# Performance work log

Measured on AMD Instinct MI355X. Metric: run time of the kernel, lower is better.

The kernel has to match this reference:

```python
import jax, jax.numpy as jnp
import numpy as np

WL_W = 8   # wl_weight
WL_IN = 8  # wl_activate (input quantization)
EPS = 1e-5

def _wq(x, bits):
    # WAGE-style uniform quantize-dequantize to `bits` bits in [-1+step, 1-step], STE passthrough
    step = 2.0 ** (1 - bits)
    q = jnp.clip(jnp.round(x / step) * step, -1.0 + step, 1.0 - step)
    return x + jax.lax.stop_gradient(q - x)

def _qconv(x, w, b, pad):
    y = jax.lax.conv_general_dilated(
        _wq(x, WL_IN), _wq(w, WL_W), (1, 1), [(pad, pad), (pad, pad)],
        dimension_numbers=('NCHW', 'OIHW', 'NCHW'))
    return y + b[None, :, None, None]

def _bn_relu(x, g, be):
    # BatchNorm2d in training mode: batch statistics over (N, H, W)
    m = jnp.mean(x, axis=(0, 2, 3), keepdims=True)
    v = jnp.var(x, axis=(0, 2, 3), keepdims=True)
    return jax.nn.relu((x - m) * jax.lax.rsqrt(v + EPS) * g[None, :, None, None] + be[None, :, None, None])

def _maxpool3(x):
    # MaxPool2d(3, stride=1, padding=1)
    return jax.lax.reduce_window(x, -jnp.inf, jax.lax.max,
                                 (1, 1, 3, 3), (1, 1, 1, 1),
                                 [(0, 0), (0, 0), (1, 1), (1, 1)])

def setup_inputs() -> dict:
    key = jax.random.key(0)
    ks = jax.random.split(key, 8)
    d = {'x': jax.random.normal(ks[0], (128, 192, 32, 32), jnp.float32)}
    specs = [('b1', 1, 64, 192, 1), ('b2a', 2, 96, 192, 1), ('b2b', 3, 128, 96, 3),
             ('b3a', 4, 16, 192, 1), ('b3b', 5, 32, 16, 3), ('b3c', 6, 32, 32, 3),
             ('b4', 7, 32, 192, 1)]
    for name, i, co, ci, k in specs:
        d[name + '_w'] = jax.random.normal(ks[i], (co, ci, k, k), jnp.float32) * 0.05
        d[name + '_b'] = jnp.zeros((co,), jnp.float32)
        d[name + '_g'] = jnp.ones((co,), jnp.float32)
        d[name + '_be'] = jnp.zeros((co,), jnp.float32)
    return d

def reference(x,
              b1_w, b1_b, b1_g, b1_be,
              b2a_w, b2a_b, b2a_g, b2a_be,
              b2b_w, b2b_b, b2b_g, b2b_be,
              b3a_w, b3a_b, b3a_g, b3a_be,
              b3b_w, b3b_b, b3b_g, b3b_be,
              b3c_w, b3c_b, b3c_g, b3c_be,
              b4_w, b4_b, b4_g, b4_be):
    y1 = _bn_relu(_qconv(x, b1_w, b1_b, 0), b1_g, b1_be)
    y2 = _bn_relu(_qconv(x, b2a_w, b2a_b, 0), b2a_g, b2a_be)
    y2 = _bn_relu(_qconv(y2, b2b_w, b2b_b, 1), b2b_g, b2b_be)
    y3 = _bn_relu(_qconv(x, b3a_w, b3a_b, 0), b3a_g, b3a_be)
    y3 = _bn_relu(_qconv(y3, b3b_w, b3b_b, 1), b3b_g, b3b_be)
    y3 = _bn_relu(_qconv(y3, b3c_w, b3c_b, 1), b3c_g, b3c_be)
    y4 = _bn_relu(_qconv(_maxpool3(x), b4_w, b4_b, 0), b4_g, b4_be)
    return jnp.concatenate([y1, y2, y3, y4], axis=1)  # [N, 256, 32, 32]
```

## Files before the change

kernel.cpp:

```cpp
#include <hip/hip_runtime.h>

typedef unsigned short u16;
typedef unsigned int u32;
typedef __attribute__((ext_vector_type(4))) int i32x4;
typedef __attribute__((ext_vector_type(4))) float f32x4;
typedef __attribute__((ext_vector_type(4))) u16 u16x4;
typedef __attribute__((ext_vector_type(8))) u16 u16x8;

#define PTOT 131072
#define NREP 16

static __device__ __forceinline__ int qi8(float v) {
  int q = (int)rintf(v * 128.f);
  return max(-127, min(127, q));
}
static __device__ __forceinline__ u16 bf_rne(float v) {
  u32 u = __float_as_uint(v);
  u += 0x7fffu + ((u >> 16) & 1u);
  return (u16)(u >> 16);
}
static __device__ __forceinline__ float bf2f(u16 v) {
  return __uint_as_float((u32)v << 16);
}

struct WPtrs { const float* p[7]; };

__global__ void wpack_kernel(WPtrs wp, char* __restrict__ o) {
  static const int S[7][5] = {
      {0,      192, 192, 1, 64},
      {12288,  192, 192, 1, 96},
      {30720,  96,  320, 3, 128},
      {153600, 192, 192, 1, 16},
      {156672, 16,  64,  3, 32},
      {162816, 32,  128, 3, 32},
      {175104, 192, 192, 1, 32},
  };
  int idx = blockIdx.x * 256 + threadIdx.x;
  if (idx >= 181248) return;
  int s = 0;
#pragma unroll
  for (int i = 1; i < 7; ++i)
    if (idx >= S[i][0]) s = i;
  int local = idx - S[s][0];
  int CIr = S[s][1], KROWP = S[s][2], KH = S[s][3], Co = S[s][4];
  int j = local & 15, lane = (local >> 4) & 63, f = local >> 10;
  int NF = Co >> 4;
  int c = f / NF, nf = f - c * NF;
  int co = nf * 16 + (lane & 15);
  int k = c * 64 + ((lane >> 4) << 4) + j;
  int r = k / KROWP, kk = k - r * KROWP;
  char val = 0;
  if (kk < 3 * CIr || KH == 1) {
    int kw = (KH == 1) ? 0 : (kk / CIr);
    int ci = (KH == 1) ? kk : (kk - kw * CIr);
    val = (char)qi8(wp.p[s][(((size_t)co * CIr + ci) * KH + r) * KH + kw]);
  }
  o[idx] = val;
}

__global__ __launch_bounds__(256) void quantx_kernel(const float* __restrict__ x,
                                                     char* __restrict__ xq) {
  __shared__ __align__(16) char tile[64][80];
  int n = blockIdx.z, hwb = blockIdx.x * 64, cb = blockIdx.y * 64;
  int lane = threadIdx.x & 63, sub = threadIdx.x >> 6;
#pragma unroll
  for (int i = 0; i < 16; ++i) {
    int c = sub + i * 4;
    float v = x[(((size_t)n * 192 + cb + c) << 10) + hwb + lane];
    tile[lane][c] = (char)qi8(v);
  }
  __syncthreads();
  int t = threadIdx.x, px = t >> 2, c16 = t & 3;
  uint4 v = *(const uint4*)&tile[px][c16 * 16];
  *(uint4*)&xq[(((size_t)n << 10) + hwb + px) * 192 + cb + c16 * 16] = v;
}

__global__ __launch_bounds__(256) void pool_kernel(const char* __restrict__ xq,
                                                   char* __restrict__ xpq) {
  int idx = blockIdx.x * 256 + threadIdx.x;
  int c16 = idx % 12;
  int p = idx / 12;
  int n = p >> 10, hw = p & 1023, h = hw >> 5, w = hw & 31;
  int m[16];
#pragma unroll
  for (int j = 0; j < 16; ++j) m[j] = -127;
  for (int dh = -1; dh <= 1; ++dh) {
    int hh = h + dh; if (hh < 0 || hh > 31) continue;
    for (int dw = -1; dw <= 1; ++dw) {
      int ww = w + dw; if (ww < 0 || ww > 31) continue;
      uint4 v = *(const uint4*)&xq[((((size_t)n << 5) + hh) * 32 + ww) * 192 + c16 * 16];
      const char* bb = reinterpret_cast<const char*>(&v);
#pragma unroll
      for (int t = 0; t < 16; ++t) {
        int b = (int)bb[t];
        m[t] = b > m[t] ? b : m[t];
      }
    }
  }
  uint4 o;
  char* ob = reinterpret_cast<char*>(&o);
#pragma unroll
  for (int t = 0; t < 16; ++t) ob[t] = (char)m[t];
  *(uint4*)&xpq[(size_t)p * 192 + c16 * 16] = o;
}

template <int NFW, int MF>
static __device__ __forceinline__ void conv_epilogue(
    i32x4 (&acc)[MF][NFW], int nfw, int lane, int wave, int mbase,
    u16* __restrict__ yh, double* __restrict__ stb, int ststride) {
  float yv[MF][NFW][4];
#pragma unroll
  for (int mf = 0; mf < MF; ++mf)
#pragma unroll
    for (int nf = 0; nf < NFW; ++nf)
      if (nf < nfw) {
        int col = nf * 16 + (lane & 15);
        int pix = mbase + mf * 16 + ((lane >> 4) << 2);
        u16x4 o;
#pragma unroll
        for (int r = 0; r < 4; ++r) {
          float v = (float)acc[mf][nf][r] * 6.103515625e-05f;
          yv[mf][nf][r] = v;
          o[r] = bf_rne(v);
        }
        *(u16x4*)&yh[(size_t)col * PTOT + pix] = o;
      }

  float s1[NFW], s2[NFW];
#pragma unroll
  for (int nf = 0; nf < NFW; ++nf) { s1[nf] = 0.f; s2[nf] = 0.f; }
#pragma unroll
  for (int mf = 0; mf < MF; ++mf)
#pragma unroll
    for (int nf = 0; nf < NFW; ++nf)
      if (nf < nfw)
#pragma unroll
        for (int r = 0; r < 4; ++r) {
          float v = yv[mf][nf][r];
          s1[nf] += v;
          s2[nf] += v * v;
        }
#pragma unroll
  for (int m = 16; m <= 32; m <<= 1)
#pragma unroll
    for (int nf = 0; nf < NFW; ++nf) {
      s1[nf] += __shfl_xor(s1[nf], m);
      s2[nf] += __shfl_xor(s2[nf], m);
    }
  __shared__ float red[4][NFW][16][2];
  if (lane < 16)
#pragma unroll
    for (int nf = 0; nf < NFW; ++nf) {
      red[wave][nf][lane][0] = s1[nf];
      red[wave][nf][lane][1] = s2[nf];
    }
  __syncthreads();
  const int t = threadIdx.x;
  if (t < 16 * nfw) {
    int nf = t >> 4, l = t & 15;
    float a = red[0][nf][l][0] + red[1][nf][l][0] + red[2][nf][l][0] + red[3][nf][l][0];
    float b = red[0][nf][l][1] + red[1][nf][l][1] + red[2][nf][l][1] + red[3][nf][l][1];
    int rep = blockIdx.x & (NREP - 1);
    atomicAdd(&stb[rep * ststride + 2 * t], (double)a);
    atomicAdd(&stb[rep * ststride + 2 * t + 1], (double)b);
  }
}

__global__ __launch_bounds__(256, 4) void cstat1x1_kernel(
    const char* __restrict__ xq, const char* __restrict__ xpq,
    const char* __restrict__ bpk, double* __restrict__ st, u16* __restrict__ yh) {
  constexpr int NFW = 6;
  constexpr int MF = 2;
  __shared__ __align__(16) char btile[18432];

  const int b = blockIdx.y;
  const int nfw = (b == 0) ? 4 : (b == 1) ? 6 : (b == 2) ? 1 : 2;
  const int bpo = (b == 0) ? 0 : (b == 1) ? 12288 : (b == 2) ? 153600 : 175104;
  const int sto = (b == 0) ? 0 : (b == 1) ? 256 * NREP
                           : (b == 2) ? 3 * 256 * NREP : 6 * 256 * NREP;
  const int yho = (b == 0) ? 0 : (b == 1) ? 64 : (b == 2) ? 160 : 176;
  const char* xin = (b == 3) ? xpq : xq;
  const char* bp = bpk + bpo;
  double* stb = st + sto;
  u16* yhb = yh + (size_t)yho * PTOT;

  const int tid = threadIdx.x;
  const int bsz = nfw * 3 * 1024;
  for (int s = tid * 16; s < bsz; s += 4096)
    *(uint4*)&btile[s] = *(const uint4*)(bp + s);
  __syncthreads();

  const int lane = tid & 63;
  const int wave = tid >> 6;
  const int mbase = blockIdx.x * 128 + wave * 32;

  uint abase[MF];
#pragma unroll
  for (int mf = 0; mf < MF; ++mf)
    abase[mf] = (uint)(mbase + mf * 16 + (lane & 15)) * 192u;
  const uint klane = (uint)(lane >> 4) * 16u;
  const uint blane = (uint)lane * 16u;

  i32x4 acc[MF][NFW];
#pragma unroll
  for (int i = 0; i < MF; ++i)
#pragma unroll
    for (int j = 0; j < NFW; ++j) acc[i][j] = {0, 0, 0, 0};

#pragma unroll
  for (int c = 0; c < 3; ++c) {
    i32x4 af[MF];
#pragma unroll
    for (int mf = 0; mf < MF; ++mf)
      af[mf] = *(const i32x4*)(xin + (abase[mf] + (uint)c * 64u + klane));
    i32x4 bfr[NFW];
#pragma unroll
    for (int nf = 0; nf < NFW; ++nf)
      if (nf < nfw)
        bfr[nf] = *(const i32x4*)&btile[(uint)((c * nfw + nf) * 1024) + blane];
#pragma unroll
    for (int mf = 0; mf < MF; ++mf)
#pragma unroll
      for (int nf = 0; nf < NFW; ++nf)
        if (nf < nfw)
          acc[mf][nf] = __builtin_amdgcn_mfma_i32_16x16x64_i8(af[mf], bfr[nf],
                                                              acc[mf][nf], 0, 0, 0);
  }

  conv_epilogue<NFW, MF>(acc, nfw, lane, wave, mbase, yhb, stb, 256);
}

template <int CI, int KROWP, int COB>
__global__ __launch_bounds__(256, 4) void cstat9q_kernel(
    const u16* __restrict__ yhin, const double* __restrict__ stp,
    const float* __restrict__ gp, const float* __restrict__ bep,
    const char* __restrict__ bp, int nft,
    double* __restrict__ stb, u16* __restrict__ yh) {
  constexpr int CPR = KROWP / 64;
  constexpr int NCH = 3 * CPR;
  constexpr int NFW = COB / 16;
  constexpr int MF = 2;
  constexpr int TILE = 6 * 34 * CI;
  constexpr int BSZ = NCH * NFW * 1024;

  __shared__ __align__(16) char atile[TILE + 64];
  __shared__ __align__(16) char btile[BSZ];
  __shared__ float2 cfl[CI];

  const int tid = threadIdx.x;

  if (tid < CI) {
    double s1d = 0., s2d = 0.;
#pragma unroll
    for (int r = 0; r < NREP; ++r) {
      s1d += stp[r * 256 + 2 * tid];
      s2d += stp[r * 256 + 2 * tid + 1];
    }
    double m = s1d * (1.0 / PTOT);
    double v = s2d * (1.0 / PTOT) - m * m;
    double inv = 1.0 / sqrt(v + 1e-5);
    double c0 = (double)gp[tid] * inv;
    cfl[tid] = make_float2((float)c0, (float)((double)bep[tid] - m * c0));
  }
  for (int s = tid * 16; s < BSZ; s += 4096)
    *(uint4*)&btile[s] = *(const uint4*)(bp + s);
  {
    uint4 z = {0, 0, 0, 0};
    for (int s = tid * 16; s < TILE + 64; s += 4096) *(uint4*)&atile[s] = z;
  }
  __syncthreads();

  const int p0 = blockIdx.x * 128;
  const int n = p0 >> 10, h0 = (p0 & 1023) >> 5;
  for (int task = tid; task < CI * 6; task += 256) {
    int co = task / 6, rr = task - co * 6;
    int irow = h0 - 1 + rr;
    if (irow < 0 || irow > 31) continue;
    const u16* src = yhin + (size_t)co * PTOT + (n << 10) + (irow << 5);
    float2 cc = cfl[co];
    char* dst = &atile[(rr * 34 + 1) * CI + co];
#pragma unroll
    for (int w8 = 0; w8 < 4; ++w8) {
      u16x8 v = *(const u16x8*)(src + w8 * 8);
#pragma unroll
      for (int e = 0; e < 8; ++e) {
        float z = fmaxf(fmaf(bf2f(v[e]), cc.x, cc.y), 0.f);
        dst[(w8 * 8 + e) * CI] = (char)min((int)rintf(z * 128.f), 127);
      }
    }
  }
  __syncthreads();

  const int lane = tid & 63;
  const int wave = tid >> 6;
  const int mbase = blockIdx.x * 128 + wave * 32;

  uint albase[MF];
#pragma unroll
  for (int mf = 0; mf < MF; ++mf) {
    int lp = wave * 32 + mf * 16 + (lane & 15);
    albase[mf] = (uint)((((lp >> 5) + 1) * 34 + 1 + (lp & 31)) * CI);
  }
  const uint klane = (uint)(lane >> 4) * 16u;
  const uint blane = (uint)lane * 16u;

  i32x4 acc[MF][NFW];
#pragma unroll
  for (int i = 0; i < MF; ++i)
#pragma unroll
    for (int j = 0; j < NFW; ++j) acc[i][j] = {0, 0, 0, 0};

#pragma unroll 2
  for (int c = 0; c < NCH; ++c) {
    int rr = c / CPR, o = (c - rr * CPR) * 64;
    uint koff = (uint)((rr - 1) * 34 * CI + o - CI);
    i32x4 af[MF];
#pragma unroll
    for (int mf = 0; mf < MF; ++mf)
      af[mf] = *(const i32x4*)&atile[albase[mf] + koff + klane];
    i32x4 bfr[NFW];
#pragma unroll
    for (int nf = 0; nf < NFW; ++nf)
      bfr[nf] = *(const i32x4*)&btile[(uint)((c * nft + nf) * 1024) + blane];
#pragma unroll
    for (int mf = 0; mf < MF; ++mf)
#pragma unroll
      for (int nf = 0; nf < NFW; ++nf)
        acc[mf][nf] = __builtin_amdgcn_mfma_i32_16x16x64_i8(af[mf], bfr[nf],
                                                            acc[mf][nf], 0, 0, 0);
  }

  conv_epilogue<NFW, MF>(acc, NFW, lane, wave, mbase, yh, stb, 256);
}

__global__ __launch_bounds__(256, 3) void cstat9q2_kernel(
    const u16* __restrict__ yhin, const double* __restrict__ stp,
    const float* __restrict__ gp, const float* __restrict__ bep,
    const char* __restrict__ bp, double* __restrict__ stb, u16* __restrict__ yh) {
  constexpr int CI = 96;
  constexpr int CPR = 5;
  constexpr int NCH = 15;
  constexpr int MF = 4;
  constexpr int NFW = 4;
  constexpr int TILE = 6 * 34 * CI;

  __shared__ __align__(16) char atile[TILE + 64];
  __shared__ float2 cfl[CI];
  __shared__ float red[4][NFW][16][2];

  const int tid = threadIdx.x;

  if (tid < CI) {
    double s1d = 0., s2d = 0.;
#pragma unroll
    for (int r = 0; r < NREP; ++r) {
      s1d += stp[r * 256 + 2 * tid];
      s2d += stp[r * 256 + 2 * tid + 1];
    }
    double m = s1d * (1.0 / PTOT);
    double v = s2d * (1.0 / PTOT) - m * m;
    double inv = 1.0 / sqrt(v + 1e-5);
    double c0 = (double)gp[tid] * inv;
    cfl[tid] = make_float2((float)c0, (float)((double)bep[tid] - m * c0));
  }
  {
    uint4 z = {0, 0, 0, 0};
    for (int s = tid * 16; s < TILE + 64; s += 4096) *(uint4*)&atile[s] = z;
  }
  __syncthreads();

  const int p0 = blockIdx.x * 128;
  const int n = p0 >> 10, h0 = (p0 & 1023) >> 5;
  for (int task = tid; task < CI * 6; task += 256) {
    int co = task / 6, rr = task - co * 6;
    int irow = h0 - 1 + rr;
    if (irow < 0 || irow > 31) continue;
    const u16* src = yhin + (size_t)co * PTOT + (n << 10) + (irow << 5);
    float2 cc = cfl[co];
    char* dst = &atile[(rr * 34 + 1) * CI + co];
#pragma unroll
    for (int w8 = 0; w8 < 4; ++w8) {
      u16x8 v = *(const u16x8*)(src + w8 * 8);
#pragma unroll
      for (int e = 0; e < 8; ++e) {
        float z = fmaxf(fmaf(bf2f(v[e]), cc.x, cc.y), 0.f);
        dst[(w8 * 8 + e) * CI] = (char)min((int)rintf(z * 128.f), 127);
      }
    }
  }
  __syncthreads();

  const int lane = tid & 63;
  const int wave = tid >> 6;
  const int pg = wave >> 1, cg = wave & 1;

  uint albase[MF];
#pragma unroll
  for (int mf = 0; mf < MF; ++mf) {
    int lp = pg * 64 + mf * 16 + (lane & 15);
    albase[mf] = (uint)((((lp >> 5) + 1) * 34 + 1 + (lp & 31)) * CI);
  }
  const uint klane = (uint)(lane >> 4) * 16u;
  const uint blane = (uint)lane * 16u;

  i32x4 acc[MF][NFW];
#pragma unroll
  for (int i = 0; i < MF; ++i)
#pragma unroll
    for (int j = 0; j < NFW; ++j) acc[i][j] = {0, 0, 0, 0};

#pragma unroll 3
  for (int c = 0; c < NCH; ++c) {
    int rr = c / CPR, o = (c - rr * CPR) * 64;
    uint koff = (uint)((rr - 1) * 34 * CI + o - CI);
    i32x4 af[MF];
#pragma unroll
    for (int mf = 0; mf < MF; ++mf)
      af[mf] = *(const i32x4*)&atile[albase[mf] + koff + klane];
    i32x4 bfr[NFW];
#pragma unroll
    for (int nf = 0; nf < NFW; ++nf)
      bfr[nf] = *(const i32x4*)(bp + ((uint)((c * 8 + cg * 4 + nf) * 1024) + blane));
#pragma unroll
    for (int mf = 0; mf < MF; ++mf)
#pragma unroll
      for (int nf = 0; nf < NFW; ++nf)
        acc[mf][nf] = __builtin_amdgcn_mfma_i32_16x16x64_i8(af[mf], bfr[nf],
                                                            acc[mf][nf], 0, 0, 0);
  }

  float yv[MF][NFW][4];
#pragma unroll
  for (int mf = 0; mf < MF; ++mf)
#pragma unroll
    for (int nf = 0; nf < NFW; ++nf) {
      int col = cg * 64 + nf * 16 + (lane & 15);
      int pix = p0 + pg * 64 + mf * 16 + ((lane >> 4) << 2);
      u16x4 o;
#pragma unroll
      for (int r = 0; r < 4; ++r) {
        float v = (float)acc[mf][nf][r] * 6.103515625e-05f;
        yv[mf][nf][r] = v;
        o[r] = bf_rne(v);
      }
      *(u16x4*)&yh[(size_t)col * PTOT + pix] = o;
    }

  float s1[NFW], s2[NFW];
#pragma unroll
  for (int nf = 0; nf < NFW; ++nf) { s1[nf] = 0.f; s2[nf] = 0.f; }
#pragma unroll
  for (int mf = 0; mf < MF; ++mf)
#pragma unroll
    for (int nf = 0; nf < NFW; ++nf)
#pragma unroll
      for (int r = 0; r < 4; ++r) {
        float v = yv[mf][nf][r];
        s1[nf] += v;
        s2[nf] += v * v;
      }
#pragma unroll
  for (int m = 16; m <= 32; m <<= 1)
#pragma unroll
    for (int nf = 0; nf < NFW; ++nf) {
      s1[nf] += __shfl_xor(s1[nf], m);
      s2[nf] += __shfl_xor(s2[nf], m);
    }
  if (lane < 16)
#pragma unroll
    for (int nf = 0; nf < NFW; ++nf) {
      red[wave][nf][lane][0] = s1[nf];
      red[wave][nf][lane][1] = s2[nf];
    }
  __syncthreads();
  if (tid < 128) {
    int gch = tid >> 4, l = tid & 15;
    int cg2 = gch >> 2, nf = gch & 3;
    float a = red[cg2][nf][l][0] + red[2 + cg2][nf][l][0];
    float b = red[cg2][nf][l][1] + red[2 + cg2][nf][l][1];
    int rep = blockIdx.x & (NREP - 1);
    atomicAdd(&stb[rep * 256 + 2 * tid], (double)a);
    atomicAdd(&stb[rep * 256 + 2 * tid + 1], (double)b);
  }
}

struct BnPtrs { const float* g[4]; const float* be[4]; };

__global__ __launch_bounds__(256) void bnout_all_kernel(
    const u16* __restrict__ yh, const double* __restrict__ st, BnPtrs bp,
    float* __restrict__ out) {
  int co = blockIdx.y, chunk = blockIdx.x, tid = threadIdx.x;
  int br = (co < 64) ? 0 : (co < 192) ? 1 : (co < 224) ? 2 : 3;
  int lco = co - ((br == 0) ? 0 : (br == 1) ? 64 : (br == 2) ? 192 : 224);
  int yhoff = (br == 0) ? 0 : (br == 1) ? 208 : (br == 2) ? 368 : 176;
  int stoff = (br == 0) ? 0 : (br == 1) ? 2 * 256 * NREP
                         : (br == 2) ? 5 * 256 * NREP : 6 * 256 * NREP;
  const double* stb = st + stoff;
  double s1d = 0., s2d = 0.;
#pragma unroll
  for (int r = 0; r < NREP; ++r) {
    s1d += stb[r * 256 + 2 * lco];
    s2d += stb[r * 256 + 2 * lco + 1];
  }
  double m = s1d * (1.0 / PTOT);
  double v = s2d * (1.0 / PTOT) - m * m;
  double inv = 1.0 / sqrt(v + 1e-5);
  double c0d = (double)bp.g[br][lco] * inv;
  float c0 = (float)c0d;
  float c1 = (float)((double)bp.be[br][lco] - m * c0d);

  int p0 = chunk * 4096 + tid * 16;
  int n = p0 >> 10, hw = p0 & 1023;
  const u16* yp = yh + (size_t)(yhoff + lco) * PTOT + p0;
  float* op = out + (((size_t)(n * 256 + co)) << 10) + hw;
#pragma unroll
  for (int half = 0; half < 2; ++half) {
    u16x8 r = *(const u16x8*)(yp + half * 8);
    f32x4 a, b;
#pragma unroll
    for (int e = 0; e < 4; ++e) {
      a[e] = fmaxf(fmaf(bf2f(r[e]), c0, c1), 0.f);
      b[e] = fmaxf(fmaf(bf2f(r[e + 4]), c0, c1), 0.f);
    }
    *(f32x4*)(op + half * 8) = a;
    *(f32x4*)(op + half * 8 + 4) = b;
  }
}

extern "C" void kernel_launch(void* const* d_in, const int* in_sizes, int n_in,
                              void* d_out, int out_size, void* d_ws, size_t ws_size,
                              hipStream_t stream) {
  const float* x = (const float*)d_in[0];
  float* out = (float*)d_out;
  char* ws = (char*)d_ws;

  if (ws_size < 155599872ull) return;
  char* xq  = ws;
  char* xpq = ws + 25165824ull;
  u16* yh   = (u16*)(ws + 50331648ull);
  char* bpk = ws + 155189248ull;
  double* st = (double*)(ws + 155370496ull);

  hipMemsetAsync(st, 0, 7 * NREP * 256 * 8, stream);

  WPtrs wp;
  const int widx[7] = {1, 5, 9, 13, 17, 21, 25};
  for (int i = 0; i < 7; ++i) wp.p[i] = (const float*)d_in[widx[i]];
  wpack_kernel<<<708, 256, 0, stream>>>(wp, bpk);

  quantx_kernel<<<dim3(16, 3, 128), 256, 0, stream>>>(x, xq);
  pool_kernel<<<6144, 256, 0, stream>>>(xq, xpq);

  double* stB[7];
  for (int b = 0; b < 7; ++b) stB[b] = st + (size_t)b * NREP * 256;

  cstat1x1_kernel<<<dim3(1024, 4), 256, 0, stream>>>(xq, xpq, bpk, st, yh);

  cstat9q2_kernel<<<1024, 256, 0, stream>>>(
      yh + (size_t)64 * PTOT, stB[1], (const float*)d_in[7], (const float*)d_in[8],
      bpk + 30720, stB[2], yh + (size_t)208 * PTOT);

  cstat9q_kernel<16, 64, 32><<<1024, 256, 0, stream>>>(
      yh + (size_t)160 * PTOT, stB[3], (const float*)d_in[15], (const float*)d_in[16],
      bpk + 156672, 2, stB[4], yh + (size_t)336 * PTOT);

  cstat9q_kernel<32, 128, 32><<<1024, 256, 0, stream>>>(
      yh + (size_t)336 * PTOT, stB[4], (const float*)d_in[19], (const float*)d_in[20],
      bpk + 162816, 2, stB[5], yh + (size_t)368 * PTOT);

  BnPtrs bp;
  bp.g[0] = (const float*)d_in[3];  bp.be[0] = (const float*)d_in[4];
  bp.g[1] = (const float*)d_in[11]; bp.be[1] = (const float*)d_in[12];
  bp.g[2] = (const float*)d_in[23]; bp.be[2] = (const float*)d_in[24];
  bp.g[3] = (const float*)d_in[27]; bp.be[3] = (const float*)d_in[28];
  bnout_all_kernel<<<dim3(32, 256), 256, 0, stream>>>(yh, st, bp, out);
}
```

Before: 193.6 us.

## Fuse maxpool into branch-4 conv and merge two 3x3 convs into one launch

Removes the standalone pool kernel and its global xpq buffer: a new cpool4 kernel computes the 3x3 max-pool of the int8 input into shared memory and runs the 1x1 branch-4 conv directly from there. The 96->128 3x3 conv and the 16->32 3x3 conv are merged into one launch with blockIdx.y picking the branch, so the two independent convs run concurrently and one launch is saved. This cuts a global write and read of the pooled tensor plus launch gaps. In exchange, the pool reads neighbours redundantly from global, and the merged kernel pairs unequal workloads under one shared-memory and register budget.

```diff
diff --git a/kernel.cpp b/kernel.cpp
--- a/kernel.cpp
+++ b/kernel.cpp
@@ -75,35 +75,6 @@
   *(uint4*)&xq[(((size_t)n << 10) + hwb + px) * 192 + cb + c16 * 16] = v;
 }
 
-__global__ __launch_bounds__(256) void pool_kernel(const char* __restrict__ xq,
-                                                   char* __restrict__ xpq) {
-  int idx = blockIdx.x * 256 + threadIdx.x;
-  int c16 = idx % 12;
-  int p = idx / 12;
-  int n = p >> 10, hw = p & 1023, h = hw >> 5, w = hw & 31;
-  int m[16];
-#pragma unroll
-  for (int j = 0; j < 16; ++j) m[j] = -127;
-  for (int dh = -1; dh <= 1; ++dh) {
-    int hh = h + dh; if (hh < 0 || hh > 31) continue;
-    for (int dw = -1; dw <= 1; ++dw) {
-      int ww = w + dw; if (ww < 0 || ww > 31) continue;
-      uint4 v = *(const uint4*)&xq[((((size_t)n << 5) + hh) * 32 + ww) * 192 + c16 * 16];
-      const char* bb = reinterpret_cast<const char*>(&v);
-#pragma unroll
-      for (int t = 0; t < 16; ++t) {
-        int b = (int)bb[t];
-        m[t] = b > m[t] ? b : m[t];
-      }
-    }
-  }
-  uint4 o;
-  char* ob = reinterpret_cast<char*>(&o);
-#pragma unroll
-  for (int t = 0; t < 16; ++t) ob[t] = (char)m[t];
-  *(uint4*)&xpq[(size_t)p * 192 + c16 * 16] = o;
-}
-
 template <int NFW, int MF>
 static __device__ __forceinline__ void conv_epilogue(
     i32x4 (&acc)[MF][NFW], int nfw, int lane, int wave, int mbase,
@@ -167,19 +138,17 @@
 }
 
 __global__ __launch_bounds__(256, 4) void cstat1x1_kernel(
-    const char* __restrict__ xq, const char* __restrict__ xpq,
-    const char* __restrict__ bpk, double* __restrict__ st, u16* __restrict__ yh) {
+    const char* __restrict__ xq, const char* __restrict__ bpk,
+    double* __restrict__ st, u16* __restrict__ yh) {
   constexpr int NFW = 6;
   constexpr int MF = 2;
   __shared__ __align__(16) char btile[18432];
 
   const int b = blockIdx.y;
-  const int nfw = (b == 0) ? 4 : (b == 1) ? 6 : (b == 2) ? 1 : 2;
-  const int bpo = (b == 0) ? 0 : (b == 1) ? 12288 : (b == 2) ? 153600 : 175104;
-  const int sto = (b == 0) ? 0 : (b == 1) ? 256 * NREP
-                           : (b == 2) ? 3 * 256 * NREP : 6 * 256 * NREP;
-  const int yho = (b == 0) ? 0 : (b == 1) ? 64 : (b == 2) ? 160 : 176;
-  const char* xin = (b == 3) ? xpq : xq;
+  const int nfw = (b == 0) ? 4 : (b == 1) ? 6 : 1;
+  const int bpo = (b == 0) ? 0 : (b == 1) ? 12288 : 153600;
+  const int sto = (b == 0) ? 0 : (b == 1) ? 256 * NREP : 3 * 256 * NREP;
+  const int yho = (b == 0) ? 0 : (b == 1) ? 64 : 160;
   const char* bp = bpk + bpo;
   double* stb = st + sto;
   u16* yhb = yh + (size_t)yho * PTOT;
@@ -212,7 +181,7 @@
     i32x4 af[MF];
 #pragma unroll
     for (int mf = 0; mf < MF; ++mf)
-      af[mf] = *(const i32x4*)(xin + (abase[mf] + (uint)c * 64u + klane));
+      af[mf] = *(const i32x4*)(xq + (abase[mf] + (uint)c * 64u + klane));
     i32x4 bfr[NFW];
 #pragma unroll
     for (int nf = 0; nf < NFW; ++nf)
@@ -228,6 +197,86 @@
   }
 
   conv_epilogue<NFW, MF>(acc, nfw, lane, wave, mbase, yhb, stb, 256);
+}
+
+__global__ __launch_bounds__(256, 4) void cpool4_kernel(
+    const char* __restrict__ xq, const char* __restrict__ bp,
+    double* __restrict__ stb, u16* __restrict__ yh) {
+  constexpr int NFW = 2;
+  constexpr int MF = 2;
+  __shared__ __align__(16) char pooled[128 * 192];
+  __shared__ __align__(16) char btile[6144];
+
+  const int tid = threadIdx.x;
+  for (int s = tid * 16; s < 6144; s += 4096)
+    *(uint4*)&btile[s] = *(const uint4*)(bp + s);
+
+  const int p0 = blockIdx.x * 128;
+  const int n = p0 >> 10, h0 = (p0 & 1023) >> 5;
+  for (int task = tid; task < 128 * 12; task += 256) {
+    int px = task / 12, c16 = task - px * 12;
+    int h = h0 + (px >> 5), w = px & 31;
+    int m[16];
+#pragma unroll
+    for (int j = 0; j < 16; ++j) m[j] = -127;
+    for (int dh = -1; dh <= 1; ++dh) {
+      int hh = h + dh; if (hh < 0 || hh > 31) continue;
+      for (int dw = -1; dw <= 1; ++dw) {
+        int ww = w + dw; if (ww < 0 || ww > 31) continue;
+        uint4 v = *(const uint4*)&xq[((size_t)((n << 10) + (hh << 5) + ww)) * 192 +
+                                     c16 * 16];
+        const char* bb = reinterpret_cast<const char*>(&v);
+#pragma unroll
+        for (int t = 0; t < 16; ++t) {
+          int b = (int)bb[t];
+          m[t] = b > m[t] ? b : m[t];
+        }
+      }
+    }
+    uint4 o;
+    char* ob = reinterpret_cast<char*>(&o);
+#pragma unroll
+    for (int t = 0; t < 16; ++t) ob[t] = (char)m[t];
+    *(uint4*)&pooled[px * 192 + c16 * 16] = o;
+  }
+  __syncthreads();
+
+  const int lane = tid & 63;
+  const int wave = tid >> 6;
+  const int mbase = blockIdx.x * 128 + wave * 32;
+
+  uint albase[MF];
+#pragma unroll
+  for (int mf = 0; mf < MF; ++mf)
+    albase[mf] = (uint)(wave * 32 + mf * 16 + (lane & 15)) * 192u;
+  const uint klane = (uint)(lane >> 4) * 16u;
+  const uint blane = (uint)lane * 16u;
+
+  i32x4 acc[MF][NFW];
+#pragma unroll
+  for (int i = 0; i < MF; ++i)
+#pragma unroll
+    for (int j = 0; j < NFW; ++j) acc[i][j] = {0, 0, 0, 0};
+
+#pragma unroll
+  for (int c = 0; c < 3; ++c) {
+    i32x4 af[MF];
+#pragma unroll
+    for (int mf = 0; mf < MF; ++mf)
+      af[mf] = *(const i32x4*)&pooled[albase[mf] + (uint)c * 64u + klane];
+    i32x4 bfr[NFW];
+#pragma unroll
+    for (int nf = 0; nf < NFW; ++nf)
+      bfr[nf] = *(const i32x4*)&btile[(uint)((c * NFW + nf) * 1024) + blane];
+#pragma unroll
+    for (int mf = 0; mf < MF; ++mf)
+#pragma unroll
+      for (int nf = 0; nf < NFW; ++nf)
+        acc[mf][nf] = __builtin_amdgcn_mfma_i32_16x16x64_i8(af[mf], bfr[nf],
+                                                            acc[mf][nf], 0, 0, 0);
+  }
+
+  conv_epilogue<NFW, MF>(acc, NFW, lane, wave, mbase, yh, stb, 256);
 }
 
 template <int CI, int KROWP, int COB>
@@ -333,154 +382,252 @@
   conv_epilogue<NFW, MF>(acc, NFW, lane, wave, mbase, yh, stb, 256);
 }
 
-__global__ __launch_bounds__(256, 3) void cstat9q2_kernel(
-    const u16* __restrict__ yhin, const double* __restrict__ stp,
-    const float* __restrict__ gp, const float* __restrict__ bep,
-    const char* __restrict__ bp, double* __restrict__ stb, u16* __restrict__ yh) {
-  constexpr int CI = 96;
-  constexpr int CPR = 5;
-  constexpr int NCH = 15;
-  constexpr int MF = 4;
-  constexpr int NFW = 4;
-  constexpr int TILE = 6 * 34 * CI;
-
-  __shared__ __align__(16) char atile[TILE + 64];
-  __shared__ float2 cfl[CI];
-  __shared__ float red[4][NFW][16][2];
+struct M2Args {
+  const u16* yhin0; const double* stp0; const float* g0; const float* be0;
+  const char* bp0; double* stb0; u16* yho0;
+  const u16* yhin1; const double* stp1; const float* g1; const float* be1;
+  const char* bp1; double* stb1; u16* yho1;
+};
+
+__global__ __launch_bounds__(256, 3) void cstat9m_kernel(M2Args A) {
+  __shared__ __align__(16) char atile[6 * 34 * 96 + 64];
+  __shared__ __align__(16) char btile[6144];
+  __shared__ float2 cfl[96];
+  __shared__ float redm[4][4][16][2];
 
   const int tid = threadIdx.x;
 
-  if (tid < CI) {
-    double s1d = 0., s2d = 0.;
-#pragma unroll
-    for (int r = 0; r < NREP; ++r) {
-      s1d += stp[r * 256 + 2 * tid];
-      s2d += stp[r * 256 + 2 * tid + 1];
-    }
-    double m = s1d * (1.0 / PTOT);
-    double v = s2d * (1.0 / PTOT) - m * m;
-    double inv = 1.0 / sqrt(v + 1e-5);
-    double c0 = (double)gp[tid] * inv;
-    cfl[tid] = make_float2((float)c0, (float)((double)bep[tid] - m * c0));
-  }
-  {
-    uint4 z = {0, 0, 0, 0};
-    for (int s = tid * 16; s < TILE + 64; s += 4096) *(uint4*)&atile[s] = z;
-  }
-  __syncthreads();
-
-  const int p0 = blockIdx.x * 128;
-  const int n = p0 >> 10, h0 = (p0 & 1023) >> 5;
-  for (int task = tid; task < CI * 6; task += 256) {
-    int co = task / 6, rr = task - co * 6;
-    int irow = h0 - 1 + rr;
-    if (irow < 0 || irow > 31) continue;
-    const u16* src = yhin + (size_t)co * PTOT + (n << 10) + (irow << 5);
-    float2 cc = cfl[co];
-    char* dst = &atile[(rr * 34 + 1) * CI + co];
-#pragma unroll
-    for (int w8 = 0; w8 < 4; ++w8) {
-      u16x8 v = *(const u16x8*)(src + w8 * 8);
-#pragma unroll
-      for (int e = 0; e < 8; ++e) {
-        float z = fmaxf(fmaf(bf2f(v[e]), cc.x, cc.y), 0.f);
-        dst[(w8 * 8 + e) * CI] = (char)min((int)rintf(z * 128.f), 127);
-      }
-    }
-  }
-  __syncthreads();
-
-  const int lane = tid & 63;
-  const int wave = tid >> 6;
-  const int pg = wave >> 1, cg = wave & 1;
-
-  uint albase[MF];
-#pragma unroll
-  for (int mf = 0; mf < MF; ++mf) {
-    int lp = pg * 64 + mf * 16 + (lane & 15);
-    albase[mf] = (uint)((((lp >> 5) + 1) * 34 + 1 + (lp & 31)) * CI);
-  }
-  const uint klane = (uint)(lane >> 4) * 16u;
-  const uint blane = (uint)lane * 16u;
-
-  i32x4 acc[MF][NFW];
-#pragma unroll
-  for (int i = 0; i < MF; ++i)
-#pragma unroll
-    for (int j = 0; j < NFW; ++j) acc[i][j] = {0, 0, 0, 0};
+  if (blockIdx.y == 0) {
+    constexpr int CI = 96;
+    constexpr int CPR = 5;
+    constexpr int NCH = 15;
+    constexpr int MF = 4;
+    constexpr int NFW = 4;
+    constexpr int TILE = 6 * 34 * CI;
+
+    if (tid < CI) {
+      double s1d = 0., s2d = 0.;
+#pragma unroll
+      for (int r = 0; r < NREP; ++r) {
+        s1d += A.stp0[r * 256 + 2 * tid];
+        s2d += A.stp0[r * 256 + 2 * tid + 1];
+      }
+      double m = s1d * (1.0 / PTOT);
+      double v = s2d * (1.0 / PTOT) - m * m;
+      double inv = 1.0 / sqrt(v + 1e-5);
+      double c0 = (double)A.g0[tid] * inv;
+      cfl[tid] = make_float2((float)c0, (float)((double)A.be0[tid] - m * c0));
+    }
+    {
+      uint4 z = {0, 0, 0, 0};
+      for (int s = tid * 16; s < TILE + 64; s += 4096) *(uint4*)&atile[s] = z;
+    }
+    __syncthreads();
+
+    const int p0 = blockIdx.x * 128;
+    const int n = p0 >> 10, h0 = (p0 & 1023) >> 5;
+    for (int task = tid; task < CI * 6; task += 256) {
+      int co = task / 6, rr = task - co * 6;
+      int irow = h0 - 1 + rr;
+      if (irow < 0 || irow > 31) continue;
+      const u16* src = A.yhin0 + (size_t)co * PTOT + (n << 10) + (irow << 5);
+      float2 cc = cfl[co];
+      char* dst = &atile[(rr * 34 + 1) * CI + co];
+#pragma unroll
+      for (int w8 = 0; w8 < 4; ++w8) {
+        u16x8 v = *(const u16x8*)(src + w8 * 8);
+#pragma unroll
+        for (int e = 0; e < 8; ++e) {
+          float z = fmaxf(fmaf(bf2f(v[e]), cc.x, cc.y), 0.f);
+          dst[(w8 * 8 + e) * CI] = (char)min((int)rintf(z * 128.f), 127);
+        }
+      }
+    }
+    __syncthreads();
+
+    const int lane = tid & 63;
+    const int wave = tid >> 6;
+    const int pg = wave >> 1, cg = wave & 1;
+
+    uint albase[MF];
+#pragma unroll
+    for (int mf = 0; mf < MF; ++mf) {
+      int lp = pg * 64 + mf * 16 + (lane & 15);
+      albase[mf] = (uint)((((lp >> 5) + 1) * 34 + 1 + (lp & 31)) * CI);
+    }
+    const uint klane = (uint)(lane >> 4) * 16u;
+    const uint blane = (uint)lane * 16u;
+
+    i32x4 acc[MF][NFW];
+#pragma unroll
+    for (int i = 0; i < MF; ++i)
+#pragma unroll
+      for (int j = 0; j < NFW; ++j) acc[i][j] = {0, 0, 0, 0};
 
 #pragma unroll 3
-  for (int c = 0; c < NCH; ++c) {
-    int rr = c / CPR, o = (c - rr * CPR) * 64;
-    uint koff = (uint)((rr - 1) * 34 * CI + o - CI);
-    i32x4 af[MF];
+    for (int c = 0; c < NCH; ++c) {
+      int rr = c / CPR, o = (c - rr * CPR) * 64;
+      uint koff = (uint)((rr - 1) * 34 * CI + o - CI);
+      i32x4 af[MF];
+#pragma unroll
+      for (int mf = 0; mf < MF; ++mf)
+        af[mf] = *(const i32x4*)&atile[albase[mf] + koff + klane];
+      i32x4 bfr[NFW];
+#pragma unroll
+      for (int nf = 0; nf < NFW; ++nf)
+        bfr[nf] = *(const i32x4*)(A.bp0 +
+                                  ((uint)((c * 8 + cg * 4 + nf) * 1024) + blane));
+#pragma unroll
+      for (int mf = 0; mf < MF; ++mf)
+#pragma unroll
+        for (int nf = 0; nf < NFW; ++nf)
+          acc[mf][nf] = __builtin_amdgcn_mfma_i32_16x16x64_i8(af[mf], bfr[nf],
+                                                              acc[mf][nf], 0, 0, 0);
+    }
+
+    float yv[MF][NFW][4];
 #pragma unroll
     for (int mf = 0; mf < MF; ++mf)
-      af[mf] = *(const i32x4*)&atile[albase[mf] + koff + klane];
-    i32x4 bfr[NFW];
-#pragma unroll
-    for (int nf = 0; nf < NFW; ++nf)
-      bfr[nf] = *(const i32x4*)(bp + ((uint)((c * 8 + cg * 4 + nf) * 1024) + blane));
+#pragma unroll
+      for (int nf = 0; nf < NFW; ++nf) {
+        int col = cg * 64 + nf * 16 + (lane & 15);
+        int pix = p0 + pg * 64 + mf * 16 + ((lane >> 4) << 2);
+        u16x4 o;
+#pragma unroll
+        for (int r = 0; r < 4; ++r) {
+          float v = (float)acc[mf][nf][r] * 6.103515625e-05f;
+          yv[mf][nf][r] = v;
+          o[r] = bf_rne(v);
+        }
+        *(u16x4*)&A.yho0[(size_t)col * PTOT + pix] = o;
+      }
+
+    float s1[NFW], s2[NFW];
+#pragma unroll
+    for (int nf = 0; nf < NFW; ++nf) { s1[nf] = 0.f; s2[nf] = 0.f; }
 #pragma unroll
     for (int mf = 0; mf < MF; ++mf)
 #pragma unroll
       for (int nf = 0; nf < NFW; ++nf)
-        acc[mf][nf] = __builtin_amdgcn_mfma_i32_16x16x64_i8(af[mf], bfr[nf],
-                                                            acc[mf][nf], 0, 0, 0);
-  }
-
-  float yv[MF][NFW][4];
-#pragma unroll
-  for (int mf = 0; mf < MF; ++mf)
-#pragma unroll
-    for (int nf = 0; nf < NFW; ++nf) {
-      int col = cg * 64 + nf * 16 + (lane & 15);
-      int pix = p0 + pg * 64 + mf * 16 + ((lane >> 4) << 2);
-      u16x4 o;
-#pragma unroll
-      for (int r = 0; r < 4; ++r) {
-        float v = (float)acc[mf][nf][r] * 6.103515625e-05f;
-        yv[mf][nf][r] = v;
-        o[r] = bf_rne(v);
-      }
-      *(u16x4*)&yh[(size_t)col * PTOT + pix] = o;
-    }
-
-  float s1[NFW], s2[NFW];
-#pragma unroll
-  for (int nf = 0; nf < NFW; ++nf) { s1[nf] = 0.f; s2[nf] = 0.f; }
-#pragma unroll
-  for (int mf = 0; mf < MF; ++mf)
-#pragma unroll
-    for (int nf = 0; nf < NFW; ++nf)
-#pragma unroll
-      for (int r = 0; r < 4; ++r) {
-        float v = yv[mf][nf][r];
-        s1[nf] += v;
-        s2[nf] += v * v;
-      }
-#pragma unroll
-  for (int m = 16; m <= 32; m <<= 1)
-#pragma unroll
-    for (int nf = 0; nf < NFW; ++nf) {
-      s1[nf] += __shfl_xor(s1[nf], m);
-      s2[nf] += __shfl_xor(s2[nf], m);
-    }
-  if (lane < 16)
-#pragma unroll
-    for (int nf = 0; nf < NFW; ++nf) {
-      red[wave][nf][lane][0] = s1[nf];
-      red[wave][nf][lane][1] = s2[nf];
-    }
-  __syncthreads();
-  if (tid < 128) {
-    int gch = tid >> 4, l = tid & 15;
-    int cg2 = gch >> 2, nf = gch & 3;
-    float a = red[cg2][nf][l][0] + red[2 + cg2][nf][l][0];
-    float b = red[cg2][nf][l][1] + red[2 + cg2][nf][l][1];
-    int rep = blockIdx.x & (NREP - 1);
-    atomicAdd(&stb[rep * 256 + 2 * tid], (double)a);
-    atomicAdd(&stb[rep * 256 + 2 * tid + 1], (double)b);
+#pragma unroll
+        for (int r = 0; r < 4; ++r) {
+          float v = yv[mf][nf][r];
+          s1[nf] += v;
+          s2[nf] += v * v;
+        }
+#pragma unroll
+    for (int m = 16; m <= 32; m <<= 1)
+#pragma unroll
+      for (int nf = 0; nf < NFW; ++nf) {
+        s1[nf] += __shfl_xor(s1[nf], m);
+        s2[nf] += __shfl_xor(s2[nf], m);
+      }
+    if (lane < 16)
+#pragma unroll
+      for (int nf = 0; nf < NFW; ++nf) {
+        redm[wave][nf][lane][0] = s1[nf];
+        redm[wave][nf][lane][1] = s2[nf];
+      }
+    __syncthreads();
+    if (tid < 128) {
+      int gch = tid >> 4, l = tid & 15;
+      int cg2 = gch >> 2, nf = gch & 3;
+      float a = redm[cg2][nf][l][0] + redm[2 + cg2][nf][l][0];
+      float b = redm[cg2][nf][l][1] + redm[2 + cg2][nf][l][1];
+      int rep = blockIdx.x & (NREP - 1);
+      atomicAdd(&A.stb0[rep * 256 + 2 * tid], (double)a);
+      atomicAdd(&A.stb0[rep * 256 + 2 * tid + 1], (double)b);
+    }
+  } else {
+    constexpr int CI = 16;
+    constexpr int CPR = 1;
+    constexpr int NCH = 3;
+    constexpr int MF = 2;
+    constexpr int NFW = 2;
+    constexpr int TILE = 6 * 34 * CI;
+
+    if (tid < CI) {
+      double s1d = 0., s2d = 0.;
+#pragma unroll
+      for (int r = 0; r < NREP; ++r) {
+        s1d += A.stp1[r * 256 + 2 * tid];
+        s2d += A.stp1[r * 256 + 2 * tid + 1];
+      }
+      double m = s1d * (1.0 / PTOT);
+      double v = s2d * (1.0 / PTOT) - m * m;
+      double inv = 1.0 / sqrt(v + 1e-5);
+      double c0 = (double)A.g1[tid] * inv;
+      cfl[tid] = make_float2((float)c0, (float)((double)A.be1[tid] - m * c0));
+    }
+    for (int s = tid * 16; s < 6144; s += 4096)
+      *(uint4*)&btile[s] = *(const uint4*)(A.bp1 + s);
+    {
+      uint4 z = {0, 0, 0, 0};
+      for (int s = tid * 16; s < TILE + 64; s += 4096) *(uint4*)&atile[s] = z;
+    }
+    __syncthreads();
+
+    const int p0 = blockIdx.x * 128;
+    const int n = p0 >> 10, h0 = (p0 & 1023) >> 5;
+    for (int task = tid; task < CI * 6; task += 256) {
+      int co = task / 6, rr = task - co * 6;
+      int irow = h0 - 1 + rr;
+      if (irow < 0 || irow > 31) continue;
+      const u16* src = A.yhin1 + (size_t)co * PTOT + (n << 10) + (irow << 5);
+      float2 cc = cfl[co];
+      char* dst = &atile[(rr * 34 + 1) * CI + co];
+#pragma unroll
+      for (int w8 = 0; w8 < 4; ++w8) {
+        u16x8 v = *(const u16x8*)(src + w8 * 8);
+#pragma unroll
+        for (int e = 0; e < 8; ++e) {
+          float z = fmaxf(fmaf(bf2f(v[e]), cc.x, cc.y), 0.f);
+          dst[(w8 * 8 + e) * CI] = (char)min((int)rintf(z * 128.f), 127);
+        }
+      }
+    }
+    __syncthreads();
+
+    const int lane = tid & 63;
+    const int wave = tid >> 6;
+    const int mbase = blockIdx.x * 128 + wave * 32;
+
+    uint albase[MF];
+#pragma unroll
+    for (int mf = 0; mf < MF; ++mf) {
+      int lp = wave * 32 + mf * 16 + (lane & 15);
+      albase[mf] = (uint)((((lp >> 5) + 1) * 34 + 1 + (lp & 31)) * CI);
+    }
+    const uint klane = (uint)(lane >> 4) * 16u;
+    const uint blane = (uint)lane * 16u;
+
+    i32x4 acc[MF][NFW];
+#pragma unroll
+    for (int i = 0; i < MF; ++i)
+#pragma unroll
+      for (int j = 0; j < NFW; ++j) acc[i][j] = {0, 0, 0, 0};
+
+#pragma unroll
+    for (int c = 0; c < NCH; ++c) {
+      int rr = c / CPR, o = (c - rr * CPR) * 64;
+      uint koff = (uint)((rr - 1) * 34 * CI + o - CI);
+      i32x4 af[MF];
+#pragma unroll
+      for (int mf = 0; mf < MF; ++mf)
+        af[mf] = *(const i32x4*)&atile[albase[mf] + koff + klane];
+      i32x4 bfr[NFW];
+#pragma unroll
+      for (int nf = 0; nf < NFW; ++nf)
+        bfr[nf] = *(const i32x4*)&btile[(uint)((c * 2 + nf) * 1024) + blane];
+#pragma unroll
+      for (int mf = 0; mf < MF; ++mf)
+#pragma unroll
+        for (int nf = 0; nf < NFW; ++nf)
+          acc[mf][nf] = __builtin_amdgcn_mfma_i32_16x16x64_i8(af[mf], bfr[nf],
+                                                              acc[mf][nf], 0, 0, 0);
+    }
+
+    conv_epilogue<NFW, MF>(acc, NFW, lane, wave, mbase, A.yho1, A.stb1, 256);
   }
 }
 
@@ -536,7 +683,6 @@
 
   if (ws_size < 155599872ull) return;
   char* xq  = ws;
-  char* xpq = ws + 25165824ull;
   u16* yh   = (u16*)(ws + 50331648ull);
   char* bpk = ws + 155189248ull;
   double* st = (double*)(ws + 155370496ull);
@@ -549,20 +695,25 @@
   wpack_kernel<<<708, 256, 0, stream>>>(wp, bpk);
 
   quantx_kernel<<<dim3(16, 3, 128), 256, 0, stream>>>(x, xq);
-  pool_kernel<<<6144, 256, 0, stream>>>(xq, xpq);
 
   double* stB[7];
   for (int b = 0; b < 7; ++b) stB[b] = st + (size_t)b * NREP * 256;
 
-  cstat1x1_kernel<<<dim3(1024, 4), 256, 0, stream>>>(xq, xpq, bpk, st, yh);
-
-  cstat9q2_kernel<<<1024, 256, 0, stream>>>(
-      yh + (size_t)64 * PTOT, stB[1], (const float*)d_in[7], (const float*)d_in[8],
-      bpk + 30720, stB[2], yh + (size_t)208 * PTOT);
-
-  cstat9q_kernel<16, 64, 32><<<1024, 256, 0, stream>>>(
-      yh + (size_t)160 * PTOT, stB[3], (const float*)d_in[15], (const float*)d_in[16],
-      bpk + 156672, 2, stB[4], yh + (size_t)336 * PTOT);
+  cpool4_kernel<<<1024, 256, 0, stream>>>(xq, bpk + 175104, stB[6],
+                                          yh + (size_t)176 * PTOT);
+
+  cstat1x1_kernel<<<dim3(1024, 3), 256, 0, stream>>>(xq, bpk, st, yh);
+
+  M2Args A;
+  A.yhin0 = yh + (size_t)64 * PTOT;  A.stp0 = stB[1];
+  A.g0 = (const float*)d_in[7];      A.be0 = (const float*)d_in[8];
+  A.bp0 = bpk + 30720;               A.stb0 = stB[2];
+  A.yho0 = yh + (size_t)208 * PTOT;
+  A.yhin1 = yh + (size_t)160 * PTOT; A.stp1 = stB[3];
+  A.g1 = (const float*)d_in[15];     A.be1 = (const float*)d_in[16];
+  A.bp1 = bpk + 156672;              A.stb1 = stB[4];
+  A.yho1 = yh + (size_t)336 * PTOT;
+  cstat9m_kernel<<<dim3(1024, 2), 256, 0, stream>>>(A);
 
   cstat9q_kernel<32, 128, 32><<<1024, 256, 0, stream>>>(
       yh + (size_t)336 * PTOT, stB[4], (const float*)d_in[19], (const float*)d_in[20],
```

Measured after the change: 186.3 us. -3.8%, faster.
